# Optimization experiments

Measured on AMD Instinct MI355X. Metric: run time of the kernel, lower is better.

The kernel has to match this reference:

```python
import jax, jax.numpy as jnp
import numpy as np
import math

HEADS = 16


def setup_inputs() -> dict:
    key = jax.random.key(0)
    kx, kq, kk, kv = jax.random.split(key, 4)
    B, S, E = 2, 2048, 1024
    x = jax.random.normal(kx, (B, S, E), dtype=jnp.float32)
    # torch nn.Linear weights are [out, in]; y = x @ W.T
    Wq = jax.random.normal(kq, (E, E), dtype=jnp.float32) * (1.0 / math.sqrt(E))
    Wk = jax.random.normal(kk, (E, E), dtype=jnp.float32) * (1.0 / math.sqrt(E))
    Wv = jax.random.normal(kv, (E, E), dtype=jnp.float32) * (1.0 / math.sqrt(E))
    # multiplicative causal mask, as the module applies mask by elementwise multiply
    mask = jnp.tril(jnp.ones((S, S), dtype=jnp.float32))
    return {"x": x, "Wq": Wq, "Wk": Wk, "Wv": Wv, "mask": mask}


def reference(x, Wq, Wk, Wv, mask):
    B, S, E = x.shape
    H = HEADS
    D = E // H
    q = (x @ Wq.T).reshape(B, S, H, D)
    k = (x @ Wk.T).reshape(B, S, H, D)
    v = (x @ Wv.T).reshape(B, S, H, D)
    # scores: [B, H, S, S]
    sim = jnp.einsum('nqhd,nkhd->nhqk', q, k)
    sim = sim * mask  # multiplicative mask, broadcast over (B, H)
    # NOTE: original scales by sqrt(emsize), not sqrt(head_dim)
    attn = jax.nn.softmax(sim / math.sqrt(E), axis=-1)
    out = jnp.einsum('nhql,nlhd->nqhd', attn, v).reshape(B, S, E)
    return out
```

## Files before the change

### kernel.cpp

```cpp
#include <hip/hip_runtime.h>
#include <hip/hip_bf16.h>
#include <cstdint>

using bf16   = __bf16;
using bf16x4 = __attribute__((ext_vector_type(4))) __bf16;
using bf16x8 = __attribute__((ext_vector_type(8))) __bf16;
using f32x4  = __attribute__((ext_vector_type(4))) float;

#define MFMA16(a, b, c) __builtin_amdgcn_mfma_f32_16x16x32_bf16((a), (b), (c), 0, 0, 0)

__device__ __forceinline__ void load_lds16(const bf16* g, bf16* l) {
    __builtin_amdgcn_global_load_lds(
        (const __attribute__((address_space(1))) void*)g,
        (__attribute__((address_space(3))) void*)l, 16, 0, 0);
}

__global__ __launch_bounds__(256) void cast_all(const float* __restrict__ x,
                                                const float* __restrict__ Wq,
                                                const float* __restrict__ Wk,
                                                const float* __restrict__ Wv,
                                                bf16* __restrict__ xb,
                                                bf16* __restrict__ wb,
                                                float qscale) {
    int i = blockIdx.x * 256 + threadIdx.x;
    const float* src; bf16* dst; int off; float scale = 1.0f;
    if (i < 1048576)      { src = x;  dst = xb;              off = i; }
    else if (i < 1310720) { src = Wq; dst = wb;              off = i - 1048576; scale = qscale; }
    else if (i < 1572864) { src = Wk; dst = wb + (1u << 20); off = i - 1310720; }
    else                  { src = Wv; dst = wb + (2u << 20); off = i - 1572864; }
    float4 v = reinterpret_cast<const float4*>(src)[off];
    bf16x4 o;
    o[0] = (bf16)(v.x * scale); o[1] = (bf16)(v.y * scale);
    o[2] = (bf16)(v.z * scale); o[3] = (bf16)(v.w * scale);
    reinterpret_cast<bf16x4*>(dst)[off] = o;
}

__global__ __launch_bounds__(256) void qkv_gemm(const bf16* __restrict__ xb,
                                                const bf16* __restrict__ wb,
                                                bf16* __restrict__ Qo,
                                                bf16* __restrict__ Ko,
                                                bf16* __restrict__ Vt) {
    const int id  = blockIdx.x;
    const int xcd = id & 7;
    const int r   = id >> 3;
    const int ntile = r >> 2;
    const int ms    = r & 3;
    const int mtile = xcd * 4 + ms;
    const int n0 = ntile * 128;
    const int m0 = mtile * 128;

    __shared__ __align__(16) bf16 SM[128 * 132];
    bf16* const As = SM;
    bf16* const Bs = SM + 128 * 64;

    const int t    = threadIdx.x;
    const int lane = t & 63;
    const int wid  = t >> 6;
    const int quad = lane >> 4;
    const int col  = lane & 15;
    const int wm   = wid & 1;
    const int wn   = wid >> 1;

    const int rsub = lane >> 3;
    const int csw  = ((lane & 7) ^ rsub) * 8;

    f32x4 acc[4][4] = {};

    const bf16* Ag = &xb[(size_t)(m0 + rsub) * 1024 + csw];
    const bf16* Bg = &wb[(size_t)(n0 + rsub) * 1024 + csw];

    for (int kc = 0; kc < 1024; kc += 64) {
        __syncthreads();
#pragma unroll
        for (int j = 0; j < 4; ++j) {
            const int c = wid * 4 + j;
            load_lds16(Ag + kc + (size_t)c * 8 * 1024, &As[c * 512]);
        }
#pragma unroll
        for (int j = 0; j < 4; ++j) {
            const int c = wid * 4 + j;
            load_lds16(Bg + kc + (size_t)c * 8 * 1024, &Bs[c * 512]);
        }
        __syncthreads();

#pragma unroll
        for (int ks = 0; ks < 2; ++ks) {
            const int ca = ((ks * 4 + quad) ^ (col & 7)) * 8;
            bf16x8 a[4], b[4];
#pragma unroll
            for (int i = 0; i < 4; ++i)
                a[i] = *reinterpret_cast<const bf16x8*>(
                    &As[(wm * 64 + i * 16 + col) * 64 + ca]);
#pragma unroll
            for (int i = 0; i < 4; ++i)
                b[i] = *reinterpret_cast<const bf16x8*>(
                    &Bs[(wn * 64 + i * 16 + col) * 64 + ca]);
#pragma unroll
            for (int mt = 0; mt < 4; ++mt)
#pragma unroll
                for (int nt = 0; nt < 4; ++nt)
                    acc[mt][nt] = MFMA16(a[mt], b[nt], acc[mt][nt]);
        }
    }

    const int w = ntile >> 3;
    __syncthreads();
    if (w == 2) {
#pragma unroll
        for (int mt = 0; mt < 4; ++mt)
#pragma unroll
            for (int nt = 0; nt < 4; ++nt)
#pragma unroll
                for (int r2 = 0; r2 < 4; ++r2) {
                    int s_local = wm * 64 + mt * 16 + quad * 4 + r2;
                    int n_local = wn * 64 + nt * 16 + col;
                    SM[n_local * 132 + s_local] = (bf16)acc[mt][nt][r2];
                }
    } else {
#pragma unroll
        for (int mt = 0; mt < 4; ++mt)
#pragma unroll
            for (int nt = 0; nt < 4; ++nt)
#pragma unroll
                for (int r2 = 0; r2 < 4; ++r2) {
                    int m_local = wm * 64 + mt * 16 + quad * 4 + r2;
                    int n_local = wn * 64 + nt * 16 + col;
                    SM[m_local * 132 + n_local] = (bf16)acc[mt][nt][r2];
                }
    }
    __syncthreads();

    const int sbase = m0 & 2047;
    const int bb16  = (m0 >> 11) * 16;
    if (w == 2) {
#pragma unroll
        for (int i = 0; i < 8; ++i) {
            int task = i * 256 + t;
            int row = task >> 4, ch = task & 15;
            int n1 = (n0 + row) & 1023;
            int hh = n1 >> 6, dd = n1 & 63;
            bf16x8 v = *reinterpret_cast<const bf16x8*>(&SM[row * 132 + ch * 8]);
            *reinterpret_cast<bf16x8*>(
                &Vt[((size_t)(bb16 + hh) * 64 + dd) * 2048 + sbase + ch * 8]) = v;
        }
    } else {
        bf16* const dst = (w == 0) ? Qo : Ko;
#pragma unroll
        for (int i = 0; i < 8; ++i) {
            int task = i * 256 + t;
            int row = task >> 4, ch = task & 15;
            int n1 = (n0 + ch * 8) & 1023;
            int hh = n1 >> 6, dd = n1 & 63;
            bf16x8 v = *reinterpret_cast<const bf16x8*>(&SM[row * 132 + ch * 8]);
            *reinterpret_cast<bf16x8*>(
                &dst[((size_t)(bb16 + hh) * 2048 + sbase + row) * 64 + dd]) = v;
        }
    }
}

__global__ __launch_bounds__(256) void tail_kernel(const bf16* __restrict__ Vt,
                                                   float* __restrict__ Tail) {
    const int bh = blockIdx.x >> 3;
    const int dg = blockIdx.x & 7;
    const bf16* Vg = Vt + (size_t)bh * 64 * 2048 + (size_t)dg * 8 * 2048;
    float* Tg = Tail + (size_t)bh * 33 * 64 + dg * 8;

    __shared__ float ts[8 * 33];
    const int tid = threadIdx.x;
    const int d  = tid >> 5;
    const int tt = tid & 31;

    const bf16* p = &Vg[(size_t)d * 2048 + tt * 64];
    float s = 0.0f;
#pragma unroll
    for (int j = 0; j < 8; ++j) {
        bf16x8 v = *reinterpret_cast<const bf16x8*>(p + j * 8);
#pragma unroll
        for (int e = 0; e < 8; ++e) s += (float)v[e];
    }
    ts[d * 33 + tt] = s;
    __syncthreads();

    if (tid < 8) {
        const int dd = tid;
        float acc = 0.0f;
        Tg[32 * 64 + dd] = 0.0f;
        for (int t2 = 31; t2 >= 1; --t2) {
            acc += ts[dd * 33 + t2];
            Tg[t2 * 64 + dd] = acc;
        }
    }
}

__global__ __launch_bounds__(256) void attn_kernel(const bf16* __restrict__ Q,
                                                   const bf16* __restrict__ K,
                                                   const bf16* __restrict__ Vt,
                                                   const float* __restrict__ Tail,
                                                   float* __restrict__ out) {
    const int bid  = blockIdx.x;
    const int work = (bid & 7) * 64 + (bid >> 3);
    const int bh   = work >> 4;
    const int x    = work & 15;
    const int b    = bh >> 4;
    const int h    = bh & 15;

    const int t    = threadIdx.x;
    const int lane = t & 63;
    const int wid  = t >> 6;
    const int quad = lane >> 4;
    const int col  = lane & 15;
    const int qh   = wid & 1;
    const int kh   = wid >> 1;

    const bf16* Qg = Q + (size_t)bh * 2048 * 64;
    const bf16* Kg = K + (size_t)bh * 2048 * 64;
    const bf16* Vg = Vt + (size_t)bh * 64 * 2048;

    __shared__ __align__(16) bf16 Ks[128 * 64];
    __shared__ __align__(16) bf16 Vs[64 * 128];
    __shared__ __align__(16) bf16 Ps[64 * 136];

    bf16x8 ones;
#pragma unroll
    for (int i = 0; i < 8; ++i) ones[i] = (bf16)1.0f;

    const int rsubK = lane >> 3;
    const int cswK  = ((lane & 7) ^ rsubK) * 8;
    const int rV    = lane >> 4;
    const int ccV   = lane & 15;

    for (int pp = 0; pp < 2; ++pp) {
        const int qt = pp == 0 ? (31 - x) : x;
        const int q0 = qt * 64;
        const int np = (qt >> 1) + 1;

        bf16x8 qf[2][2];
#pragma unroll
        for (int qs = 0; qs < 2; ++qs)
#pragma unroll
            for (int ks = 0; ks < 2; ++ks)
                qf[qs][ks] = *reinterpret_cast<const bf16x8*>(
                    &Qg[(size_t)(q0 + qh * 32 + qs * 16 + col) * 64 + ks * 32 + quad * 8]);

        f32x4 o[2][2];
        f32x4 la[2];
        {
            const float tc = 64.0f * (float)(32 - 2 * np);
#pragma unroll
            for (int qs = 0; qs < 2; ++qs)
#pragma unroll
                for (int r = 0; r < 4; ++r) la[qs][r] = tc;
            const float* Tg = Tail + ((size_t)bh * 33 + 2 * np) * 64;
#pragma unroll
            for (int dt = 0; dt < 2; ++dt) {
                float tv = Tg[kh * 32 + dt * 16 + col];
#pragma unroll
                for (int qs = 0; qs < 2; ++qs)
#pragma unroll
                    for (int r = 0; r < 4; ++r) o[qs][dt][r] = tv;
            }
        }

        const int s0max = (np - 1) * 128;

        for (int s0 = 0; s0 < np * 128; s0 += 128) {
            __syncthreads();
#pragma unroll
            for (int jj = 0; jj < 4; ++jj) {
                const int c = wid * 4 + jj;
                load_lds16(&Kg[(size_t)(s0 + c * 8 + rsubK) * 64 + cswK], &Ks[c * 512]);
                const int d = c * 4 + rV;
                load_lds16(&Vg[(size_t)d * 2048 + s0 + ((ccV ^ (d & 15)) * 8)], &Vs[c * 512]);
            }
            __syncthreads();

            f32x4 sv[2][4] = {};
            __builtin_amdgcn_s_setprio(1);
#pragma unroll
            for (int ks = 0; ks < 2; ++ks) {
                const int ca = ((ks * 4 + quad) ^ (col & 7)) * 8;
#pragma unroll
                for (int nt = 0; nt < 4; ++nt) {
                    bf16x8 kb = *reinterpret_cast<const bf16x8*>(
                        &Ks[((kh * 4 + nt) * 16 + col) * 64 + ca]);
                    sv[0][nt] = MFMA16(kb, qf[0][ks], sv[0][nt]);
                    sv[1][nt] = MFMA16(kb, qf[1][ks], sv[1][nt]);
                }
            }
            __builtin_amdgcn_s_setprio(0);

            if (s0 == s0max) {
#pragma unroll
                for (int qs = 0; qs < 2; ++qs) {
                    const int qc = q0 + qh * 32 + qs * 16 + col;
#pragma unroll
                    for (int nt = 0; nt < 4; ++nt)
#pragma unroll
                        for (int r = 0; r < 4; ++r) {
                            int kidx = s0 + kh * 64 + nt * 16 + quad * 4 + r;
                            if (kidx > qc) sv[qs][nt][r] = 0.0f;
                        }
                }
            }

#pragma unroll
            for (int qs = 0; qs < 2; ++qs) {
                bf16* Pq = &Ps[(qh * 32 + qs * 16 + col) * 136 + kh * 64];
#pragma unroll
                for (int nt = 0; nt < 4; ++nt) {
                    bf16x4 pw;
#pragma unroll
                    for (int r = 0; r < 4; ++r)
                        pw[r] = (bf16)__builtin_amdgcn_exp2f(sv[qs][nt][r]);
                    *reinterpret_cast<bf16x4*>(&Pq[nt * 16 + quad * 4]) = pw;
                }
            }

            __syncthreads();

            __builtin_amdgcn_s_setprio(1);
#pragma unroll
            for (int kg = 0; kg < 4; ++kg) {
                bf16x8 pa0 = *reinterpret_cast<const bf16x8*>(
                    &Ps[(qh * 32 + col) * 136 + kg * 32 + quad * 8]);
                bf16x8 pa1 = *reinterpret_cast<const bf16x8*>(
                    &Ps[(qh * 32 + 16 + col) * 136 + kg * 32 + quad * 8]);
                la[0] = MFMA16(pa0, ones, la[0]);
                la[1] = MFMA16(pa1, ones, la[1]);
#pragma unroll
                for (int dt = 0; dt < 2; ++dt) {
                    bf16x8 vb = *reinterpret_cast<const bf16x8*>(
                        &Vs[(kh * 32 + dt * 16 + col) * 128 + ((kg * 4 + quad) ^ col) * 8]);
                    o[0][dt] = MFMA16(pa0, vb, o[0][dt]);
                    o[1][dt] = MFMA16(pa1, vb, o[1][dt]);
                }
            }
            __builtin_amdgcn_s_setprio(0);
        }

#pragma unroll
        for (int qs = 0; qs < 2; ++qs) {
#pragma unroll
            for (int r = 0; r < 4; ++r) {
                int q = q0 + qh * 32 + qs * 16 + quad * 4 + r;
                float inv = __builtin_amdgcn_rcpf(la[qs][r]);
#pragma unroll
                for (int dt = 0; dt < 2; ++dt) {
                    int d = kh * 32 + dt * 16 + col;
                    out[((size_t)b * 2048 + q) * 1024 + h * 64 + d] = o[qs][dt][r] * inv;
                }
            }
        }
    }
}

extern "C" void kernel_launch(void* const* d_in, const int* in_sizes, int n_in,
                              void* d_out, int out_size, void* d_ws, size_t ws_size,
                              hipStream_t stream) {
    const float* x  = (const float*)d_in[0];
    const float* Wq = (const float*)d_in[1];
    const float* Wk = (const float*)d_in[2];
    const float* Wv = (const float*)d_in[3];
    float* out = (float*)d_out;

    char* ws = (char*)d_ws;
    bf16*  xb   = (bf16*)(ws);
    bf16*  wb   = (bf16*)(ws + (size_t)(8  << 20));
    bf16*  Qb   = (bf16*)(ws + (size_t)(14 << 20));
    bf16*  Kb   = (bf16*)(ws + (size_t)(22 << 20));
    bf16*  Vtb  = (bf16*)(ws + (size_t)(30 << 20));
    float* Tail = (float*)(ws + (size_t)(38 << 20));

    const float QSCALE = 1.44269504088896f / 32.0f;

    cast_all<<<7168, 256, 0, stream>>>(x, Wq, Wk, Wv, xb, wb, QSCALE);

    qkv_gemm<<<768, 256, 0, stream>>>(xb, wb, Qb, Kb, Vtb);

    tail_kernel<<<256, 256, 0, stream>>>(Vtb, Tail);

    attn_kernel<<<512, 256, 0, stream>>>(Qb, Kb, Vtb, Tail, out);
}
```

Before: 152.7 us.

## Split PV by key halves per wave, drop mid-loop barrier, reduce partials via LDS

In the attention kernel, each wave now writes its own P tile into a private LDS region and accumulates PV over all 64 head dims for its own key half. This removes the __syncthreads between the softmax write and the PV MFMAs. The two key-half partial outputs and row sums are combined through LDS once after the KV loop, at the cost of more accumulator registers and an epilogue reduction. Separately, cast_all becomes a grid-stride loop launched with 4x fewer blocks.

```diff
diff --git a/kernel.cpp b/kernel.cpp
--- a/kernel.cpp
+++ b/kernel.cpp
@@ -22,17 +22,18 @@
                                                 bf16* __restrict__ xb,
                                                 bf16* __restrict__ wb,
                                                 float qscale) {
-    int i = blockIdx.x * 256 + threadIdx.x;
-    const float* src; bf16* dst; int off; float scale = 1.0f;
-    if (i < 1048576)      { src = x;  dst = xb;              off = i; }
-    else if (i < 1310720) { src = Wq; dst = wb;              off = i - 1048576; scale = qscale; }
-    else if (i < 1572864) { src = Wk; dst = wb + (1u << 20); off = i - 1310720; }
-    else                  { src = Wv; dst = wb + (2u << 20); off = i - 1572864; }
-    float4 v = reinterpret_cast<const float4*>(src)[off];
-    bf16x4 o;
-    o[0] = (bf16)(v.x * scale); o[1] = (bf16)(v.y * scale);
-    o[2] = (bf16)(v.z * scale); o[3] = (bf16)(v.w * scale);
-    reinterpret_cast<bf16x4*>(dst)[off] = o;
+    for (int i = blockIdx.x * 256 + threadIdx.x; i < 1835008; i += 1792 * 256) {
+        const float* src; bf16* dst; int off; float scale = 1.0f;
+        if (i < 1048576)      { src = x;  dst = xb;              off = i; }
+        else if (i < 1310720) { src = Wq; dst = wb;              off = i - 1048576; scale = qscale; }
+        else if (i < 1572864) { src = Wk; dst = wb + (1u << 20); off = i - 1310720; }
+        else                  { src = Wv; dst = wb + (2u << 20); off = i - 1572864; }
+        float4 v = reinterpret_cast<const float4*>(src)[off];
+        bf16x4 o;
+        o[0] = (bf16)(v.x * scale); o[1] = (bf16)(v.y * scale);
+        o[2] = (bf16)(v.z * scale); o[3] = (bf16)(v.w * scale);
+        reinterpret_cast<bf16x4*>(dst)[off] = o;
+    }
 }
 
 __global__ __launch_bounds__(256) void qkv_gemm(const bf16* __restrict__ xb,
@@ -218,7 +219,8 @@
 
     __shared__ __align__(16) bf16 Ks[128 * 64];
     __shared__ __align__(16) bf16 Vs[64 * 128];
-    __shared__ __align__(16) bf16 Ps[64 * 136];
+    __shared__ __align__(16) bf16 Ps[4 * 32 * 72];
+    bf16* Pw = &Ps[wid * 32 * 72];
 
     bf16x8 ones;
 #pragma unroll
@@ -242,18 +244,18 @@
                 qf[qs][ks] = *reinterpret_cast<const bf16x8*>(
                     &Qg[(size_t)(q0 + qh * 32 + qs * 16 + col) * 64 + ks * 32 + quad * 8]);
 
-        f32x4 o[2][2];
+        f32x4 o[2][4];
         f32x4 la[2];
         {
-            const float tc = 64.0f * (float)(32 - 2 * np);
+            const float tc = (kh == 0) ? 64.0f * (float)(32 - 2 * np) : 0.0f;
 #pragma unroll
             for (int qs = 0; qs < 2; ++qs)
 #pragma unroll
                 for (int r = 0; r < 4; ++r) la[qs][r] = tc;
             const float* Tg = Tail + ((size_t)bh * 33 + 2 * np) * 64;
 #pragma unroll
-            for (int dt = 0; dt < 2; ++dt) {
-                float tv = Tg[kh * 32 + dt * 16 + col];
+            for (int dt = 0; dt < 4; ++dt) {
+                float tv = (kh == 0) ? Tg[dt * 16 + col] : 0.0f;
 #pragma unroll
                 for (int qs = 0; qs < 2; ++qs)
 #pragma unroll
@@ -305,7 +307,7 @@
 
 #pragma unroll
             for (int qs = 0; qs < 2; ++qs) {
-                bf16* Pq = &Ps[(qh * 32 + qs * 16 + col) * 136 + kh * 64];
+                bf16* Pq = &Pw[(qs * 16 + col) * 72];
 #pragma unroll
                 for (int nt = 0; nt < 4; ++nt) {
                     bf16x4 pw;
@@ -316,21 +318,20 @@
                 }
             }
 
-            __syncthreads();
-
             __builtin_amdgcn_s_setprio(1);
 #pragma unroll
-            for (int kg = 0; kg < 4; ++kg) {
+            for (int kg = 0; kg < 2; ++kg) {
+                const int g = kh * 2 + kg;
                 bf16x8 pa0 = *reinterpret_cast<const bf16x8*>(
-                    &Ps[(qh * 32 + col) * 136 + kg * 32 + quad * 8]);
+                    &Pw[(col) * 72 + kg * 32 + quad * 8]);
                 bf16x8 pa1 = *reinterpret_cast<const bf16x8*>(
-                    &Ps[(qh * 32 + 16 + col) * 136 + kg * 32 + quad * 8]);
+                    &Pw[(16 + col) * 72 + kg * 32 + quad * 8]);
                 la[0] = MFMA16(pa0, ones, la[0]);
                 la[1] = MFMA16(pa1, ones, la[1]);
 #pragma unroll
-                for (int dt = 0; dt < 2; ++dt) {
+                for (int dt = 0; dt < 4; ++dt) {
                     bf16x8 vb = *reinterpret_cast<const bf16x8*>(
-                        &Vs[(kh * 32 + dt * 16 + col) * 128 + ((kg * 4 + quad) ^ col) * 8]);
+                        &Vs[(dt * 16 + col) * 128 + ((g * 4 + quad) ^ col) * 8]);
                     o[0][dt] = MFMA16(pa0, vb, o[0][dt]);
                     o[1][dt] = MFMA16(pa1, vb, o[1][dt]);
                 }
@@ -338,16 +339,47 @@
             __builtin_amdgcn_s_setprio(0);
         }
 
-#pragma unroll
-        for (int qs = 0; qs < 2; ++qs) {
-#pragma unroll
-            for (int r = 0; r < 4; ++r) {
-                int q = q0 + qh * 32 + qs * 16 + quad * 4 + r;
-                float inv = __builtin_amdgcn_rcpf(la[qs][r]);
-#pragma unroll
-                for (int dt = 0; dt < 2; ++dt) {
-                    int d = kh * 32 + dt * 16 + col;
-                    out[((size_t)b * 2048 + q) * 1024 + h * 64 + d] = o[qs][dt][r] * inv;
+        __syncthreads();
+        {
+            float* S = reinterpret_cast<float*>(qh == 0 ? (bf16*)Ks : (bf16*)Vs);
+            if (kh == 1) {
+                float* p = S + lane * 40;
+#pragma unroll
+                for (int qs = 0; qs < 2; ++qs) {
+#pragma unroll
+                    for (int dt = 0; dt < 4; ++dt)
+                        *reinterpret_cast<f32x4*>(p + (qs * 4 + dt) * 4) = o[qs][dt];
+                    *reinterpret_cast<f32x4*>(p + 32 + qs * 4) = la[qs];
+                }
+            }
+            __syncthreads();
+            if (kh == 0) {
+                const float* p = S + lane * 40;
+#pragma unroll
+                for (int qs = 0; qs < 2; ++qs) {
+#pragma unroll
+                    for (int dt = 0; dt < 4; ++dt) {
+                        f32x4 ov = *reinterpret_cast<const f32x4*>(p + (qs * 4 + dt) * 4);
+#pragma unroll
+                        for (int r = 0; r < 4; ++r) o[qs][dt][r] += ov[r];
+                    }
+                    f32x4 lv = *reinterpret_cast<const f32x4*>(p + 32 + qs * 4);
+#pragma unroll
+                    for (int r = 0; r < 4; ++r) la[qs][r] += lv[r];
+                }
+#pragma unroll
+                for (int qs = 0; qs < 2; ++qs) {
+#pragma unroll
+                    for (int r = 0; r < 4; ++r) {
+                        int q = q0 + qh * 32 + qs * 16 + quad * 4 + r;
+                        float inv = __builtin_amdgcn_rcpf(la[qs][r]);
+#pragma unroll
+                        for (int dt = 0; dt < 4; ++dt) {
+                            int d = dt * 16 + col;
+                            out[((size_t)b * 2048 + q) * 1024 + h * 64 + d] =
+                                o[qs][dt][r] * inv;
+                        }
+                    }
                 }
             }
         }
@@ -373,7 +405,7 @@
 
     const float QSCALE = 1.44269504088896f / 32.0f;
 
-    cast_all<<<7168, 256, 0, stream>>>(x, Wq, Wk, Wv, xb, wb, QSCALE);
+    cast_all<<<1792, 256, 0, stream>>>(x, Wq, Wk, Wv, xb, wb, QSCALE);
 
     qkv_gemm<<<768, 256, 0, stream>>>(xb, wb, Qb, Kb, Vtb);
 
```

Result: no change. 155.3 us (+1.7%).
